# Kernel optimization log

Hardware: AMD Instinct MI355X
Metric: run time of the kernel (lower is better)

## Reference

```python
import jax, jax.numpy as jnp
import numpy as np

EPS = 1e-5
CLIP = 1.0

@jax.custom_vjp
def ste_sign(x):
    return jnp.sign(x)

def _ste_fwd(x):
    return jnp.sign(x), x

def _ste_bwd(x, g):
    return (g * (jnp.abs(x) <= CLIP).astype(g.dtype),)

ste_sign.defvjp(_ste_fwd, _ste_bwd)

def conv2d(x, w, stride, pad):
    return jax.lax.conv_general_dilated(
        x, w, window_strides=(stride, stride), padding=[(pad, pad), (pad, pad)],
        dimension_numbers=('NCHW', 'OIHW', 'NCHW'))

def bn(x, g, b, m, v):
    inv = g / jnp.sqrt(v + EPS)
    return x * inv[None, :, None, None] + (b - m * inv)[None, :, None, None]

def setup_inputs() -> dict:
    key = jax.random.key(0)
    ks = jax.random.split(key, 16)
    def rn(k, shape, scale=0.05):
        return jax.random.normal(k, shape, dtype=jnp.float32) * scale
    C = [64, 128, 128, 192, 192]
    d = {}
    d['x'] = jax.random.normal(ks[0], (128, 1, 128, 128), dtype=jnp.float32)
    d['conv1_w'] = rn(ks[1], (C[0], 1, 3, 3), 0.3)
    d['conv1_b'] = rn(ks[2], (C[0],))
    d['w2'] = rn(ks[3], (C[1], C[0], 3, 3), 0.3)
    d['w3'] = rn(ks[4], (C[2], C[1], 3, 3), 0.3)
    d['w4'] = rn(ks[5], (C[3], C[2], 3, 3), 0.3)
    d['w5'] = rn(ks[6], (C[4], C[3], 1, 1), 0.3)
    d['conv6_w'] = rn(ks[7], (12, C[4], 1, 1), 0.1)
    d['conv6_b'] = rn(ks[8], (12,))
    d['fc_w'] = rn(ks[9], (12, 12), 0.2)
    d['fc_b'] = rn(ks[10], (12,))
    for i, c in enumerate(C):
        kk = jax.random.split(jax.random.fold_in(key, 100 + i), 4)
        d[f'bn{i+1}_g'] = 1.0 + rn(kk[0], (c,), 0.1)
        d[f'bn{i+1}_b'] = rn(kk[1], (c,), 0.1)
        d[f'bn{i+1}_m'] = rn(kk[2], (c,), 0.1)
        d[f'bn{i+1}_v'] = 1.0 + jnp.abs(rn(kk[3], (c,), 0.1))
    return d

def reference(x, conv1_w, conv1_b, w2, w3, w4, w5, conv6_w, conv6_b, fc_w, fc_b,
              bn1_g, bn1_b, bn1_m, bn1_v, bn2_g, bn2_b, bn2_m, bn2_v,
              bn3_g, bn3_b, bn3_m, bn3_v, bn4_g, bn4_b, bn4_m, bn4_v,
              bn5_g, bn5_b, bn5_m, bn5_v):
    # conv1 (float) + BN + ReLU
    h = conv2d(x, conv1_w, 2, 1) + conv1_b[None, :, None, None]
    h = jax.nn.relu(bn(h, bn1_g, bn1_b, bn1_m, bn1_v))
    # binarized conv blocks: sign(activation) conv sign(weight)
    h = conv2d(ste_sign(h), ste_sign(w2), 1, 1)
    h = jax.nn.relu(bn(h, bn2_g, bn2_b, bn2_m, bn2_v))
    h = conv2d(ste_sign(h), ste_sign(w3), 2, 1)
    h = jax.nn.relu(bn(h, bn3_g, bn3_b, bn3_m, bn3_v))
    h = conv2d(ste_sign(h), ste_sign(w4), 1, 1)
    h = jax.nn.relu(bn(h, bn4_g, bn4_b, bn4_m, bn4_v))
    h = conv2d(ste_sign(h), ste_sign(w5), 1, 0)
    h = jax.nn.relu(bn(h, bn5_g, bn5_b, bn5_m, bn5_v))
    # 1x1 conv to classes, global average pool, FC, softmax
    h = conv2d(h, conv6_w, 1, 0) + conv6_b[None, :, None, None]
    h = jnp.mean(h, axis=(2, 3))  # [B, num_classes]
    logits = h @ fc_w.T + fc_b
    return jax.nn.softmax(logits, axis=1)
```

## Files before the change

### kernel.cpp

```cpp
#include <hip/hip_runtime.h>
#include <cstdint>

using u64 = unsigned long long;
using u32 = unsigned int;
typedef __attribute__((ext_vector_type(4))) int int4v;
typedef __attribute__((ext_vector_type(16))) int int16v;

struct PrepArgs {
  const float* bng[5]; const float* bnb[5]; const float* bnm[5]; const float* bnv[5];
  float* inv1; float* cc1; float* inv5; float* cc5;
  int* thr[3]; int* flp[3];
  const float* w[4];
  u64* wp[4]; u64* wz[4];
  u32* flags;
  const float* x; float* xpad;
  signed char* bf2x; signed char* bf3; signed char* bf4;
};

__device__ __forceinline__ void prep_all_body(const PrepArgs& a, int i) {
  if (i < 704) {
    const int off[6] = {0, 64, 192, 320, 512, 704};
    int l = 0;
    while (i >= off[l + 1]) ++l;
    int c = i - off[l];
    float iv = __fdiv_rn(a.bng[l][c], __fsqrt_rn(__fadd_rn(a.bnv[l][c], 1e-5f)));
    float cb = __fsub_rn(a.bnb[l][c], __fmul_rn(a.bnm[l][c], iv));
    if (l == 0) { a.inv1[c] = iv; a.cc1[c] = cb; }
    else if (l == 4) { a.inv5[c] = iv; a.cc5[c] = cb; }
    else {
      auto pred = [&](int v_) {
        return __fadd_rn(__fmul_rn((float)v_, iv), cb) > 0.f;
      };
      int Tx, fl;
      if (iv == 0.f) { Tx = pred(0) ? -100000 : 100000; fl = 0; }
      else if (iv > 0.f) {
        if (pred(-2048)) { Tx = -100000; fl = 0; }
        else if (!pred(2048)) { Tx = 100000; fl = 0; }
        else {
          int lo = -2048, hi = 2048;
          while (hi - lo > 1) { int md = (lo + hi) >> 1; if (pred(md)) hi = md; else lo = md; }
          Tx = hi; fl = 0;
        }
      } else {
        if (pred(2048)) { Tx = -100000; fl = -1; }
        else if (!pred(-2048)) { Tx = 100000; fl = -1; }
        else {
          int lo = -2048, hi = 2048;
          while (hi - lo > 1) { int md = (lo + hi) >> 1; if (pred(md)) lo = md; else hi = md; }
          Tx = lo ^ -1; fl = -1;
        }
      }
      a.thr[l - 1][c] = Tx; a.flp[l - 1][c] = fl;
    }
    return;
  }
  int j = i - 704;
  if (j >= 7488) return;
  const int poff[5] = {0, 1152, 3456, 6912, 7488};
  const int ICt[4] = {64, 128, 128, 192};
  const int Kt[4]  = {9, 9, 9, 1};
  const int Wt[4]  = {1, 2, 2, 3};
  int l = 0;
  while (j >= poff[l + 1]) ++l;
  int idx = j - poff[l];
  int W = Wt[l], K = Kt[l], IC = ICt[l];
  int wi = idx % W;
  int rest = idx / W;
  int t = rest % K;
  int oc = rest / K;
  u64 p = 0, z = 0;
  int icbase = wi * 64;
  int nb = IC - icbase; if (nb > 64) nb = 64;
  const float* w = a.w[l];
  for (int b = 0; b < nb; ++b) {
    float f = w[((size_t)oc * IC + (icbase + b)) * K + t];
    if (f > 0.f) p |= (1ull << b);
    else if (f == 0.f) z |= (1ull << b);
  }
  a.wp[l][idx] = p;
  a.wz[l][idx] = z;
  if (z) atomicOr(a.flags + l, 1u);
}

template <int CINW, int COUT>
__device__ __forceinline__ void prep_bfrag_body(const float* __restrict__ w,
                                                signed char* __restrict__ bf, int idx) {
  constexpr int NKC = 9 * CINW;
  constexpr int NT = COUT / 16;
  constexpr int CIN = 64 * CINW;
  if (idx >= NT * NKC * 64) return;
  int lane = idx & 63;
  int rest = idx >> 6;
  int kc = rest % NKC;
  int t = rest / NKC;
  int tap = kc / CINW, wd = kc % CINW;
  int n = t * 16 + (lane & 15);
  int icb = wd * 64 + (lane >> 4) * 16;
  signed char* dst = bf + (size_t)idx * 16;
#pragma unroll
  for (int i = 0; i < 16; ++i) {
    float f = w[((size_t)n * CIN + icb + i) * 9 + tap];
    dst[i] = (f > 0.f) ? 1 : ((f < 0.f) ? -1 : 0);
  }
}

__device__ __forceinline__ void prep_bfrag32_body(const float* __restrict__ w,
                                                  signed char* __restrict__ bf, int idx) {
  if (idx >= 4 * 18 * 64) return;
  int lane = idx & 63;
  int rest = idx >> 6;
  int s = rest % 18;
  int t = rest / 18;
  int oc = t * 32 + (lane & 31);
  int kbase = s * 32 + (lane >> 5) * 16;
  signed char* dst = bf + (size_t)idx * 16;
#pragma unroll
  for (int i = 0; i < 16; ++i) {
    int k = kbase + i;
    int ch = k & 63, tap = k >> 6;
    float f = w[((size_t)oc * 64 + ch) * 9 + tap];
    dst[i] = (f > 0.f) ? 1 : ((f < 0.f) ? -1 : 0);
  }
}

__global__ __launch_bounds__(256) void front(PrepArgs a) {
  int b = blockIdx.x, tid = threadIdx.x;
  if (b < 8192) {
    int idx = b * 256 + tid;
    int c = idx & 127, r = (idx >> 7) & 127, n = idx >> 14;
    a.xpad[((size_t)n * 130 + r + 1) * 136 + c + 1] = a.x[idx];
    return;
  }
  b -= 8192;
  if (b < 32) { prep_all_body(a, b * 256 + tid); return; }
  b -= 32;
  if (b < 18) { prep_bfrag32_body(a.w[0], a.bf2x, b * 256 + tid); return; }
  b -= 18;
  if (b < 36) { prep_bfrag_body<2, 128>(a.w[1], a.bf3, b * 256 + tid); return; }
  b -= 36;
  if (b < 54) { prep_bfrag_body<2, 192>(a.w[2], a.bf4, b * 256 + tid); return; }
}

__global__ __launch_bounds__(256) void conv1_bin(
    const float* __restrict__ xpad, const float* __restrict__ w1, const float* __restrict__ b1,
    const float* __restrict__ inv1, const float* __restrict__ cc1,
    u64* __restrict__ a1p) {
  int tid = threadIdx.x, lane = tid & 63;
  int rb = __builtin_amdgcn_readfirstlane(tid >> 6);
  int blk = blockIdx.x;
  int y = (blk % 16) * 4 + rb;
  int n = blk / 16;
  float W[9];
#pragma unroll
  for (int t = 0; t < 9; ++t) W[t] = w1[lane * 9 + t];
  float bias = b1[lane], iv = inv1[lane], cb = cc1[lane];
  const float* sb = xpad + ((size_t)n * 130 + 2 * y) * 136;
  float A[12], B[12], C[12];
  u64 rowm = 0;
  int xb = 0;

#define FLD(BUF, POFF)                                     \
  _Pragma("unroll") for (int _r = 0; _r < 3; ++_r)         \
  _Pragma("unroll") for (int _j = 0; _j < 4; ++_j)         \
    BUF[_r * 4 + _j] = sb[_r * 136 + (POFF) + _j];
#define FPX(XO, B0F, C0, B1F, C1, B2F, C2) {                          \
  float acc = 0.f;                                                    \
  _Pragma("unroll") for (int _r = 0; _r < 3; ++_r)                    \
    acc += B0F[_r * 4 + (C0)] * W[_r * 3 + 0]                         \
         + B1F[_r * 4 + (C1)] * W[_r * 3 + 1]                         \
         + B2F[_r * 4 + (C2)] * W[_r * 3 + 2];                        \
  float h = __fadd_rn(acc, bias);                                     \
  float bnv = __fadd_rn(__fmul_rn(h, iv), cb);                        \
  u64 _m = __ballot(bnv > 0.f);                                       \
  rowm = (lane == (XO)) ? _m : rowm; }
#define FSTEP(BA, BB, BC, POFF, XB)  \
  FLD(BC, (POFF) + 8);               \
  FPX((XB), BA, 0, BA, 1, BA, 2);    \
  FPX((XB) + 1, BA, 2, BA, 3, BB, 0);

  FLD(A, 0); FLD(B, 4);
  for (int g = 0; g < 10; ++g) {
    FSTEP(A, B, C, 0, xb);
    FSTEP(B, C, A, 4, xb + 2);
    FSTEP(C, A, B, 8, xb + 4);
    sb += 12; xb += 6;
  }
  FSTEP(A, B, C, 0, xb);
  FSTEP(B, C, A, 4, xb + 2);
  a1p[((size_t)n * 66 + (y + 1)) * 68 + lane + 1] = rowm;
#undef FLD
#undef FPX
#undef FSTEP
}

__global__ __launch_bounds__(256, 4) void bconv2_32(
    const u64* __restrict__ ain, const signed char* __restrict__ bf,
    const int* __restrict__ thr, const int* __restrict__ flp,
    u64* __restrict__ aout) {
  __shared__ int4v bs[2 * 18 * 64];
  int tid = threadIdx.x, lane = tid & 63;
  int wv = __builtin_amdgcn_readfirstlane(tid >> 6);
  int pos = blockIdx.x * 4 + wv;
  int xg = pos & 1;
  int y = (pos >> 1) & 63;
  int n = pos >> 7;
  int ln31 = lane & 31;
  int kg16 = (lane >> 5) * 16;
  int px = xg * 32 + ln31;

  const int4v* bfv = (const int4v*)bf;
  int4v breg[9];
#pragma unroll
  for (int i = 0; i < 9; ++i) breg[i] = bfv[tid + i * 256];

  const u64* abase = ain + ((size_t)n * 66 + y) * 68 + px;
  int4v af[18];
#pragma unroll
  for (int tap = 0; tap < 9; ++tap) {
    int dy = tap / 3, dx = tap % 3;
    u64 aw = abase[(size_t)dy * 68 + dx];
#pragma unroll
    for (int h = 0; h < 2; ++h) {
      u32 t16 = (u32)(aw >> (h * 32 + kg16)) & 0xFFFFu;
      int4v v;
      v.x = (int)((((t16      ) & 0xFu) * 0x00204081u) & 0x01010101u);
      v.y = (int)((((t16 >> 4 ) & 0xFu) * 0x00204081u) & 0x01010101u);
      v.z = (int)((((t16 >> 8 ) & 0xFu) * 0x00204081u) & 0x01010101u);
      v.w = (int)((((t16 >> 12) & 0xFu) * 0x00204081u) & 0x01010101u);
      af[tap * 2 + h] = v;
    }
  }

  int txv[4], flv[4];
#pragma unroll
  for (int t = 0; t < 4; ++t) { txv[t] = thr[t * 32 + ln31]; flv[t] = flp[t * 32 + ln31]; }

  u32* out32 = (u32*)aout;

#define C2_EPI(T, CREG) {                                             \
  int tx = txv[T], fl = flv[T];                                       \
  u32 oww = 0;                                                        \
  _Pragma("unroll") for (int r = 0; r < 16; ++r) {                    \
    int plo = (r & 3) + 8 * (r >> 2);                                 \
    u64 bal = __ballot((CREG[r] ^ fl) >= tx);                         \
    u32 wlo = (u32)bal, whi = (u32)(bal >> 32);                       \
    oww = (lane == plo) ? wlo : oww;                                  \
    oww = (lane == plo + 4) ? whi : oww;                              \
  }                                                                   \
  if (lane < 32) {                                                    \
    int xx = xg * 32 + lane;                                          \
    out32[(((size_t)n * 66 + (y + 1)) * 68 + (xx + 1)) * 4 + (T)] = oww; \
  } }

#pragma unroll
  for (int i = 0; i < 9; ++i) bs[tid + i * 256] = breg[i];
  __syncthreads();
#pragma unroll
  for (int i = 0; i < 9; ++i) breg[i] = bfv[2 * 18 * 64 + tid + i * 256];

#pragma unroll
  for (int t = 0; t < 2; ++t) {
    int16v c = {0, 0, 0, 0, 0, 0, 0, 0, 0, 0, 0, 0, 0, 0, 0, 0};
#pragma unroll
    for (int s = 0; s < 18; ++s) {
      int4v bb = bs[(t * 18 + s) * 64 + lane];
      c = __builtin_amdgcn_mfma_i32_32x32x32_i8(af[s], bb, c, 0, 0, 0);
    }
    C2_EPI(t, c)
  }

  __syncthreads();
#pragma unroll
  for (int i = 0; i < 9; ++i) bs[tid + i * 256] = breg[i];
  __syncthreads();
#pragma unroll
  for (int t = 2; t < 4; ++t) {
    int16v c = {0, 0, 0, 0, 0, 0, 0, 0, 0, 0, 0, 0, 0, 0, 0, 0};
#pragma unroll
    for (int s = 0; s < 18; ++s) {
      int4v bb = bs[((t - 2) * 18 + s) * 64 + lane];
      c = __builtin_amdgcn_mfma_i32_32x32x32_i8(af[s], bb, c, 0, 0, 0);
    }
    C2_EPI(t, c)
  }
#undef C2_EPI
}

template <int CINW, int COUT, int STRIDE, int IN_HW, int OUT_HW, int MT, int TSTG, int OPAD>
__global__ __launch_bounds__(256) void bconv_mfma(
    const u64* __restrict__ ain, const signed char* __restrict__ bf,
    const int* __restrict__ thr, const int* __restrict__ flp,
    u64* __restrict__ aout) {
  constexpr int IPW = IN_HW + 4;
  constexpr int NKC = 9 * CINW;
  constexpr int NT = COUT / 16;
  constexpr int NSTG = NT / TSTG;
  constexpr int OCW = (COUT + 63) / 64;
  constexpr int XG = OUT_HW / (16 * MT);
  constexpr int FRAG = TSTG * NKC * 64;
  constexpr int CPT = (FRAG + 255) / 256;
  constexpr int NW32 = NT / 2;
  __shared__ int4v bs[FRAG];

  int tid = threadIdx.x, lane = tid & 63;
  int wv = __builtin_amdgcn_readfirstlane(tid >> 6);
  int pos = blockIdx.x * 4 + wv;
  int xg = pos % XG;
  int rest = pos / XG;
  int y = rest % OUT_HW;
  int n = rest / OUT_HW;
  int m = lane & 15;
  int kg = lane >> 4;

  const int4v* bfv = (const int4v*)bf;

  int4v breg[CPT];
#pragma unroll
  for (int i = 0; i < CPT; ++i) {
    int ix = tid + i * 256;
    if (FRAG % 256 == 0 || ix < FRAG) breg[i] = bfv[ix];
  }

  int4v af[MT * NKC];
#pragma unroll
  for (int mt = 0; mt < MT; ++mt) {
    int x = (xg * MT + mt) * 16 + m;
    const u64* abase = ain + (((size_t)n * (IN_HW + 2) + STRIDE * y) * IPW
                              + (size_t)STRIDE * x) * CINW;
#pragma unroll
    for (int dy = 0; dy < 3; ++dy)
#pragma unroll
      for (int dx = 0; dx < 3; ++dx)
#pragma unroll
        for (int wd = 0; wd < CINW; ++wd) {
          u64 aw = abase[((size_t)dy * IPW + dx) * CINW + wd];
          u32 t16 = (u32)(aw >> (kg * 16)) & 0xFFFFu;
          int4v v;
          v.x = (int)((((t16      ) & 0xFu) * 0x00204081u) & 0x01010101u);
          v.y = (int)((((t16 >> 4 ) & 0xFu) * 0x00204081u) & 0x01010101u);
          v.z = (int)((((t16 >> 8 ) & 0xFu) * 0x00204081u) & 0x01010101u);
          v.w = (int)((((t16 >> 12) & 0xFu) * 0x00204081u) & 0x01010101u);
          af[mt * NKC + (dy * 3 + dx) * CINW + wd] = v;
        }
  }

  u32 acc32[MT][NW32];
#pragma unroll
  for (int mt = 0; mt < MT; ++mt)
#pragma unroll
    for (int wl = 0; wl < NW32; ++wl) acc32[mt][wl] = 0;

#pragma unroll
  for (int s = 0; s < NSTG; ++s) {
    __syncthreads();
#pragma unroll
    for (int i = 0; i < CPT; ++i) {
      int ix = tid + i * 256;
      if (FRAG % 256 == 0 || ix < FRAG) bs[ix] = breg[i];
    }
    __syncthreads();
    if (s + 1 < NSTG) {
      const int4v* src = bfv + (size_t)(s + 1) * FRAG;
#pragma unroll
      for (int i = 0; i < CPT; ++i) {
        int ix = tid + i * 256;
        if (FRAG % 256 == 0 || ix < FRAG) breg[i] = src[ix];
      }
    }
#pragma unroll
    for (int tl = 0; tl < TSTG; ++tl) {
      int4v c[MT];
#pragma unroll
      for (int mt = 0; mt < MT; ++mt) c[mt] = (int4v){0, 0, 0, 0};
#pragma unroll
      for (int kc = 0; kc < NKC; ++kc) {
        int4v bb = bs[(tl * NKC + kc) * 64 + lane];
#pragma unroll
        for (int mt = 0; mt < MT; ++mt)
          c[mt] = __builtin_amdgcn_mfma_i32_16x16x64_i8(af[mt * NKC + kc], bb, c[mt], 0, 0, 0);
      }
      const int t = s * TSTG + tl;
      int tx = thr[t * 16 + m];
      int fl = flp[t * 16 + m];
#pragma unroll
      for (int mt = 0; mt < MT; ++mt) {
        u64 b0 = __ballot((c[mt].x ^ fl) >= tx);
        u64 b1 = __ballot((c[mt].y ^ fl) >= tx);
        u64 b2 = __ballot((c[mt].z ^ fl) >= tx);
        u64 b3 = __ballot((c[mt].w ^ fl) >= tx);
        u64 s01 = (m & 1) ? b1 : b0;
        u64 s23 = (m & 1) ? b3 : b2;
        u64 bsel = (m & 2) ? s23 : s01;
        u32 slice = (u32)(bsel >> ((m >> 2) * 16)) & 0xFFFFu;
        acc32[mt][t >> 1] |= slice << ((t & 1) * 16);
      }
    }
  }

  if (kg == 0) {
    u32* out32 = (u32*)aout;
#pragma unroll
    for (int mt = 0; mt < MT; ++mt) {
      int x = (xg * MT + mt) * 16 + m;
      size_t px32;
      if (OPAD)
        px32 = (((size_t)n * (OUT_HW + 2) + (y + 1)) * (OUT_HW + 4) + (x + 1)) * (OCW * 2);
      else
        px32 = (((size_t)n * OUT_HW + y) * OUT_HW + x) * (OCW * 2);
#pragma unroll
      for (int wl = 0; wl < NW32; ++wl)
        out32[px32 + wl] = acc32[mt][wl];
    }
  }
}

#define NCH5 8
__global__ __launch_bounds__(192) void bconv5_pool(
    const u64* __restrict__ ain, const u64* __restrict__ wp, const u64* __restrict__ wz,
    const u32* __restrict__ flag, const float* __restrict__ inv5, const float* __restrict__ cc5,
    float* __restrict__ partial) {
  int n = blockIdx.x / NCH5, ch = blockIdx.x % NCH5;
  int oc = threadIdx.x;
  u64 W0 = wp[oc * 3], W1 = wp[oc * 3 + 1], W2 = wp[oc * 3 + 2];
  bool anyz = (*flag != 0u);
  float iv = inv5[oc], cb = cc5[oc];
  const u64* sb = ain + ((size_t)n * 1024 + ch * 128) * 3;
  u64 A0, A1, A2, B0, B1, B2, C0, C1, C2;
  float acc = 0.f;
#define LD5(P, a0_, a1_, a2_) { a0_ = sb[(P) * 3]; a1_ = sb[(P) * 3 + 1]; a2_ = sb[(P) * 3 + 2]; }
#define PX5(a0_, a1_, a2_) {                                                   \
  int _pa = __popcll(a0_) + __popcll(a1_) + __popcll(a2_);                     \
  int _s = __popcll(a0_ & W0) + __popcll(a1_ & W1) + __popcll(a2_ & W2);       \
  int _val = 2 * _s - _pa;                                                     \
  if (anyz) _val += __popcll(a0_ & wz[oc * 3]) + __popcll(a1_ & wz[oc * 3 + 1])\
                  + __popcll(a2_ & wz[oc * 3 + 2]);                            \
  float _b = __fadd_rn(__fmul_rn((float)_val, iv), cb);                        \
  acc += fmaxf(_b, 0.f); }
  LD5(0, A0, A1, A2); LD5(1, B0, B1, B2);
  for (int g = 0; g < 42; ++g) {
    LD5(2, C0, C1, C2); PX5(A0, A1, A2);
    LD5(3, A0, A1, A2); PX5(B0, B1, B2);
    LD5(4, B0, B1, B2); PX5(C0, C1, C2);
    sb += 9;
  }
  PX5(A0, A1, A2); PX5(B0, B1, B2);
  partial[((size_t)n * NCH5 + ch) * 192 + oc] = acc;
#undef LD5
#undef PX5
}

__global__ __launch_bounds__(192) void head2(
    const float* __restrict__ partial,
    const float* __restrict__ w6, const float* __restrict__ b6,
    const float* __restrict__ fw, const float* __restrict__ fb,
    float* __restrict__ out) {
  __shared__ float pool_s[192];
  __shared__ float h6s[12];
  __shared__ float lgs[12];
  int n = blockIdx.x, t = threadIdx.x;
  float s = 0.f;
#pragma unroll
  for (int ch = 0; ch < NCH5; ++ch) s += partial[((size_t)n * NCH5 + ch) * 192 + t];
  pool_s[t] = s;
  __syncthreads();
  if (t < 12) {
    float a = 0.f;
    for (int c = 0; c < 192; ++c) a += pool_s[c] * w6[t * 192 + c];
    h6s[t] = b6[t] + a * (1.0f / 1024.0f);
  }
  __syncthreads();
  if (t < 12) {
    float s2 = fb[t];
    for (int k = 0; k < 12; ++k) s2 += h6s[k] * fw[t * 12 + k];
    lgs[t] = s2;
  }
  __syncthreads();
  if (t == 0) {
    float mx = -1e30f;
    for (int j = 0; j < 12; ++j) mx = fmaxf(mx, lgs[j]);
    float e[12], se = 0.f;
    for (int j = 0; j < 12; ++j) { e[j] = expf(lgs[j] - mx); se += e[j]; }
    for (int j = 0; j < 12; ++j) out[n * 12 + j] = e[j] / se;
  }
}

extern "C" void kernel_launch(void* const* d_in, const int* in_sizes, int n_in,
                              void* d_out, int out_size, void* d_ws, size_t ws_size,
                              hipStream_t stream) {
  const float* x   = (const float*)d_in[0];
  const float* w1  = (const float*)d_in[1];
  const float* b1  = (const float*)d_in[2];
  const float* w2  = (const float*)d_in[3];
  const float* w3  = (const float*)d_in[4];
  const float* w4  = (const float*)d_in[5];
  const float* w5  = (const float*)d_in[6];
  const float* w6  = (const float*)d_in[7];
  const float* b6  = (const float*)d_in[8];
  const float* fcw = (const float*)d_in[9];
  const float* fcb = (const float*)d_in[10];
  float* out = (float*)d_out;

  char* ws = (char*)d_ws;
  size_t off = 0;
  auto alloc = [&](size_t bytes) -> void* {
    void* p = ws + off;
    off += (bytes + 255) & ~(size_t)255;
    return p;
  };
  size_t xp_sz = (size_t)128 * 130 * 136 * 4;
  size_t a1_sz = (size_t)128 * 66 * 68 * 1 * 8;
  size_t a2_sz = (size_t)128 * 66 * 68 * 2 * 8;
  size_t a3_sz = (size_t)128 * 34 * 36 * 2 * 8;
  float* xpad = (float*)alloc(xp_sz);
  u64* a1p = (u64*)alloc(a1_sz);
  u64* a2p = (u64*)alloc(a2_sz);
  u64* a3p = (u64*)alloc(a3_sz);
  size_t zero_sz = xp_sz + a1_sz + a2_sz + a3_sz;
  u64* a4p = (u64*)alloc((size_t)128 * 32 * 32 * 3 * 8);
  float* partial = (float*)alloc((size_t)128 * NCH5 * 192 * 4);
  float* inv1 = (float*)alloc(64 * 4);
  float* cc1  = (float*)alloc(64 * 4);
  float* inv5 = (float*)alloc(192 * 4);
  float* cc5  = (float*)alloc(192 * 4);
  int* thr2 = (int*)alloc(128 * 4); int* flp2 = (int*)alloc(128 * 4);
  int* thr3 = (int*)alloc(128 * 4); int* flp3 = (int*)alloc(128 * 4);
  int* thr4 = (int*)alloc(192 * 4); int* flp4 = (int*)alloc(192 * 4);
  u64* wp2 = (u64*)alloc(128 * 9 * 1 * 8);
  u64* wz2 = (u64*)alloc(128 * 9 * 1 * 8);
  u64* wp3 = (u64*)alloc(128 * 9 * 2 * 8);
  u64* wz3 = (u64*)alloc(128 * 9 * 2 * 8);
  u64* wp4 = (u64*)alloc(192 * 9 * 2 * 8);
  u64* wz4 = (u64*)alloc(192 * 9 * 2 * 8);
  u64* wp5 = (u64*)alloc(192 * 1 * 3 * 8);
  u64* wz5 = (u64*)alloc(192 * 1 * 3 * 8);
  u32* flags = (u32*)alloc(4 * sizeof(u32));
  signed char* bf2x = (signed char*)alloc((size_t)4 * 18 * 64 * 16);
  signed char* bf3 = (signed char*)alloc((size_t)8 * 18 * 64 * 16);
  signed char* bf4 = (signed char*)alloc((size_t)12 * 18 * 64 * 16);
  (void)ws_size; (void)n_in; (void)in_sizes; (void)out_size;

  hipMemsetAsync(xpad, 0, zero_sz, stream);
  hipMemsetAsync(flags, 0, 4 * sizeof(u32), stream);

  PrepArgs pa;
  for (int l = 0; l < 5; ++l) {
    pa.bng[l] = (const float*)d_in[11 + 4 * l + 0];
    pa.bnb[l] = (const float*)d_in[11 + 4 * l + 1];
    pa.bnm[l] = (const float*)d_in[11 + 4 * l + 2];
    pa.bnv[l] = (const float*)d_in[11 + 4 * l + 3];
  }
  pa.inv1 = inv1; pa.cc1 = cc1; pa.inv5 = inv5; pa.cc5 = cc5;
  pa.thr[0] = thr2; pa.flp[0] = flp2;
  pa.thr[1] = thr3; pa.flp[1] = flp3;
  pa.thr[2] = thr4; pa.flp[2] = flp4;
  pa.w[0] = w2; pa.w[1] = w3; pa.w[2] = w4; pa.w[3] = w5;
  pa.wp[0] = wp2; pa.wp[1] = wp3; pa.wp[2] = wp4; pa.wp[3] = wp5;
  pa.wz[0] = wz2; pa.wz[1] = wz3; pa.wz[2] = wz4; pa.wz[3] = wz5;
  pa.flags = flags;
  pa.x = x; pa.xpad = xpad;
  pa.bf2x = bf2x; pa.bf3 = bf3; pa.bf4 = bf4;

  front<<<8192 + 32 + 18 + 36 + 54, 256, 0, stream>>>(pa);

  conv1_bin<<<128 * 16, 256, 0, stream>>>(xpad, w1, b1, inv1, cc1, a1p);

  bconv2_32<<<4096, 256, 0, stream>>>(a1p, bf2x, thr2, flp2, a2p);

  bconv_mfma<2, 128, 2, 64, 32, 1, 1, 1><<<2048, 256, 0, stream>>>(
      a2p, bf3, thr3, flp3, a3p);

  bconv_mfma<2, 192, 1, 32, 32, 1, 1, 0><<<2048, 256, 0, stream>>>(
      a3p, bf4, thr4, flp4, a4p);

  bconv5_pool<<<128 * NCH5, 192, 0, stream>>>(a4p, wp5, wz5, flags + 3, inv5, cc5, partial);

  head2<<<128, 192, 0, stream>>>(partial, w6, b6, fcw, fcb, out);
}
```

Measured before the change: 201.3 us.

## Switch conv3/conv4 to 32x32x32 int8 MFMA with double-buffered weight tiles

Replaces the 16x16x64 MFMA binary conv kernel for layers 3 and 4 with a 32x32x32 int8 MFMA kernel where each wave handles a full 32-pixel output row. The weight fragments are repacked into a new 32-wide layout and staged through double-buffered shared memory, one output tile per iteration. The epilogue packs the ballot-based binarisation into 32-bit words per tile. This halves the block count and aims to improve MFMA efficiency and reuse of activation fragments, at the cost of more registers (36 A fragments) and a larger shared buffer that may reduce occupancy.

```diff
diff --git a/kernel.cpp b/kernel.cpp
--- a/kernel.cpp
+++ b/kernel.cpp
@@ -82,28 +82,6 @@
   if (z) atomicOr(a.flags + l, 1u);
 }
 
-template <int CINW, int COUT>
-__device__ __forceinline__ void prep_bfrag_body(const float* __restrict__ w,
-                                                signed char* __restrict__ bf, int idx) {
-  constexpr int NKC = 9 * CINW;
-  constexpr int NT = COUT / 16;
-  constexpr int CIN = 64 * CINW;
-  if (idx >= NT * NKC * 64) return;
-  int lane = idx & 63;
-  int rest = idx >> 6;
-  int kc = rest % NKC;
-  int t = rest / NKC;
-  int tap = kc / CINW, wd = kc % CINW;
-  int n = t * 16 + (lane & 15);
-  int icb = wd * 64 + (lane >> 4) * 16;
-  signed char* dst = bf + (size_t)idx * 16;
-#pragma unroll
-  for (int i = 0; i < 16; ++i) {
-    float f = w[((size_t)n * CIN + icb + i) * 9 + tap];
-    dst[i] = (f > 0.f) ? 1 : ((f < 0.f) ? -1 : 0);
-  }
-}
-
 __device__ __forceinline__ void prep_bfrag32_body(const float* __restrict__ w,
                                                   signed char* __restrict__ bf, int idx) {
   if (idx >= 4 * 18 * 64) return;
@@ -123,6 +101,27 @@
   }
 }
 
+template <int COUT>
+__device__ __forceinline__ void prep_bfrag32b_body(const float* __restrict__ w,
+                                                   signed char* __restrict__ bf, int idx) {
+  constexpr int NT = COUT / 32;
+  if (idx >= NT * 36 * 64) return;
+  int lane = idx & 63;
+  int rest = idx >> 6;
+  int s = rest % 36;
+  int t = rest / 36;
+  int oc = t * 32 + (lane & 31);
+  int kbase = s * 32 + (lane >> 5) * 16;
+  signed char* dst = bf + (size_t)idx * 16;
+#pragma unroll
+  for (int i = 0; i < 16; ++i) {
+    int k = kbase + i;
+    int ch = k % 128, tap = k / 128;
+    float f = w[((size_t)oc * 128 + ch) * 9 + tap];
+    dst[i] = (f > 0.f) ? 1 : ((f < 0.f) ? -1 : 0);
+  }
+}
+
 __global__ __launch_bounds__(256) void front(PrepArgs a) {
   int b = blockIdx.x, tid = threadIdx.x;
   if (b < 8192) {
@@ -136,9 +135,9 @@
   b -= 32;
   if (b < 18) { prep_bfrag32_body(a.w[0], a.bf2x, b * 256 + tid); return; }
   b -= 18;
-  if (b < 36) { prep_bfrag_body<2, 128>(a.w[1], a.bf3, b * 256 + tid); return; }
+  if (b < 36) { prep_bfrag32b_body<128>(a.w[1], a.bf3, b * 256 + tid); return; }
   b -= 36;
-  if (b < 54) { prep_bfrag_body<2, 192>(a.w[2], a.bf4, b * 256 + tid); return; }
+  if (b < 54) { prep_bfrag32b_body<192>(a.w[2], a.bf4, b * 256 + tid); return; }
 }
 
 __global__ __launch_bounds__(256) void conv1_bin(
@@ -286,131 +285,86 @@
 #undef C2_EPI
 }
 
-template <int CINW, int COUT, int STRIDE, int IN_HW, int OUT_HW, int MT, int TSTG, int OPAD>
-__global__ __launch_bounds__(256) void bconv_mfma(
+template <int COUT, int STRIDE, int IN_HW, int OPAD>
+__global__ __launch_bounds__(256) void bconv34_32(
     const u64* __restrict__ ain, const signed char* __restrict__ bf,
     const int* __restrict__ thr, const int* __restrict__ flp,
     u64* __restrict__ aout) {
   constexpr int IPW = IN_HW + 4;
-  constexpr int NKC = 9 * CINW;
-  constexpr int NT = COUT / 16;
-  constexpr int NSTG = NT / TSTG;
-  constexpr int OCW = (COUT + 63) / 64;
-  constexpr int XG = OUT_HW / (16 * MT);
-  constexpr int FRAG = TSTG * NKC * 64;
-  constexpr int CPT = (FRAG + 255) / 256;
-  constexpr int NW32 = NT / 2;
-  __shared__ int4v bs[FRAG];
-
+  constexpr int NT = COUT / 32;
+  constexpr int TW = 36 * 64;
+  constexpr int OW32 = COUT / 32;
+  __shared__ int4v bs[2][TW];
   int tid = threadIdx.x, lane = tid & 63;
   int wv = __builtin_amdgcn_readfirstlane(tid >> 6);
   int pos = blockIdx.x * 4 + wv;
-  int xg = pos % XG;
-  int rest = pos / XG;
-  int y = rest % OUT_HW;
-  int n = rest / OUT_HW;
-  int m = lane & 15;
-  int kg = lane >> 4;
+  int y = pos & 31;
+  int n = pos >> 5;
+  int ln31 = lane & 31;
+  int h = lane >> 5;
 
   const int4v* bfv = (const int4v*)bf;
 
-  int4v breg[CPT];
-#pragma unroll
-  for (int i = 0; i < CPT; ++i) {
-    int ix = tid + i * 256;
-    if (FRAG % 256 == 0 || ix < FRAG) breg[i] = bfv[ix];
-  }
-
-  int4v af[MT * NKC];
-#pragma unroll
-  for (int mt = 0; mt < MT; ++mt) {
-    int x = (xg * MT + mt) * 16 + m;
-    const u64* abase = ain + (((size_t)n * (IN_HW + 2) + STRIDE * y) * IPW
-                              + (size_t)STRIDE * x) * CINW;
-#pragma unroll
-    for (int dy = 0; dy < 3; ++dy)
-#pragma unroll
-      for (int dx = 0; dx < 3; ++dx)
-#pragma unroll
-        for (int wd = 0; wd < CINW; ++wd) {
-          u64 aw = abase[((size_t)dy * IPW + dx) * CINW + wd];
-          u32 t16 = (u32)(aw >> (kg * 16)) & 0xFFFFu;
-          int4v v;
-          v.x = (int)((((t16      ) & 0xFu) * 0x00204081u) & 0x01010101u);
-          v.y = (int)((((t16 >> 4 ) & 0xFu) * 0x00204081u) & 0x01010101u);
-          v.z = (int)((((t16 >> 8 ) & 0xFu) * 0x00204081u) & 0x01010101u);
-          v.w = (int)((((t16 >> 12) & 0xFu) * 0x00204081u) & 0x01010101u);
-          af[mt * NKC + (dy * 3 + dx) * CINW + wd] = v;
-        }
-  }
-
-  u32 acc32[MT][NW32];
-#pragma unroll
-  for (int mt = 0; mt < MT; ++mt)
-#pragma unroll
-    for (int wl = 0; wl < NW32; ++wl) acc32[mt][wl] = 0;
-
-#pragma unroll
-  for (int s = 0; s < NSTG; ++s) {
+  const u64* abase = ain + (((size_t)n * (IN_HW + 2) + (size_t)STRIDE * y) * IPW
+                            + (size_t)STRIDE * ln31) * 2;
+  int4v af[36];
+#pragma unroll
+  for (int tap = 0; tap < 9; ++tap) {
+    int dy = tap / 3, dx = tap % 3;
+    u64 w0 = abase[((size_t)dy * IPW + dx) * 2 + 0];
+    u64 w1 = abase[((size_t)dy * IPW + dx) * 2 + 1];
+#pragma unroll
+    for (int q = 0; q < 4; ++q) {
+      int m2 = 2 * q + h;
+      u64 aw = (m2 & 4) ? w1 : w0;
+      int sh = (m2 & 3) * 16;
+      u32 t16 = (u32)(aw >> sh) & 0xFFFFu;
+      int4v v;
+      v.x = (int)((((t16      ) & 0xFu) * 0x00204081u) & 0x01010101u);
+      v.y = (int)((((t16 >> 4 ) & 0xFu) * 0x00204081u) & 0x01010101u);
+      v.z = (int)((((t16 >> 8 ) & 0xFu) * 0x00204081u) & 0x01010101u);
+      v.w = (int)((((t16 >> 12) & 0xFu) * 0x00204081u) & 0x01010101u);
+      af[tap * 4 + q] = v;
+    }
+  }
+
+#pragma unroll
+  for (int i = 0; i < 9; ++i) bs[0][tid + i * 256] = bfv[tid + i * 256];
+  __syncthreads();
+
+  u32* out32 = (u32*)aout;
+  size_t px32;
+  if (OPAD)
+    px32 = (((size_t)n * 34 + (y + 1)) * 36 + (ln31 + 1)) * OW32;
+  else
+    px32 = (((size_t)n * 32 + y) * 32 + ln31) * OW32;
+
+#pragma unroll 1
+  for (int t = 0; t < NT; ++t) {
+    if (t + 1 < NT) {
+      const int4v* src = bfv + (size_t)(t + 1) * TW;
+#pragma unroll
+      for (int i = 0; i < 9; ++i) bs[(t + 1) & 1][tid + i * 256] = src[tid + i * 256];
+    }
+    int16v c = {0, 0, 0, 0, 0, 0, 0, 0, 0, 0, 0, 0, 0, 0, 0, 0};
+#pragma unroll
+    for (int s = 0; s < 36; ++s) {
+      int4v bb = bs[t & 1][s * 64 + lane];
+      c = __builtin_amdgcn_mfma_i32_32x32x32_i8(af[s], bb, c, 0, 0, 0);
+    }
+    int tx = thr[t * 32 + ln31];
+    int fl = flp[t * 32 + ln31];
+    u32 oww = 0;
+#pragma unroll
+    for (int r = 0; r < 16; ++r) {
+      int plo = (r & 3) + 8 * (r >> 2);
+      u64 bal = __ballot((c[r] ^ fl) >= tx);
+      u32 wlo = (u32)bal, whi = (u32)(bal >> 32);
+      oww = (lane == plo) ? wlo : oww;
+      oww = (lane == plo + 4) ? whi : oww;
+    }
+    if (lane < 32) out32[px32 + t] = oww;
     __syncthreads();
-#pragma unroll
-    for (int i = 0; i < CPT; ++i) {
-      int ix = tid + i * 256;
-      if (FRAG % 256 == 0 || ix < FRAG) bs[ix] = breg[i];
-    }
-    __syncthreads();
-    if (s + 1 < NSTG) {
-      const int4v* src = bfv + (size_t)(s + 1) * FRAG;
-#pragma unroll
-      for (int i = 0; i < CPT; ++i) {
-        int ix = tid + i * 256;
-        if (FRAG % 256 == 0 || ix < FRAG) breg[i] = src[ix];
-      }
-    }
-#pragma unroll
-    for (int tl = 0; tl < TSTG; ++tl) {
-      int4v c[MT];
-#pragma unroll
-      for (int mt = 0; mt < MT; ++mt) c[mt] = (int4v){0, 0, 0, 0};
-#pragma unroll
-      for (int kc = 0; kc < NKC; ++kc) {
-        int4v bb = bs[(tl * NKC + kc) * 64 + lane];
-#pragma unroll
-        for (int mt = 0; mt < MT; ++mt)
-          c[mt] = __builtin_amdgcn_mfma_i32_16x16x64_i8(af[mt * NKC + kc], bb, c[mt], 0, 0, 0);
-      }
-      const int t = s * TSTG + tl;
-      int tx = thr[t * 16 + m];
-      int fl = flp[t * 16 + m];
-#pragma unroll
-      for (int mt = 0; mt < MT; ++mt) {
-        u64 b0 = __ballot((c[mt].x ^ fl) >= tx);
-        u64 b1 = __ballot((c[mt].y ^ fl) >= tx);
-        u64 b2 = __ballot((c[mt].z ^ fl) >= tx);
-        u64 b3 = __ballot((c[mt].w ^ fl) >= tx);
-        u64 s01 = (m & 1) ? b1 : b0;
-        u64 s23 = (m & 1) ? b3 : b2;
-        u64 bsel = (m & 2) ? s23 : s01;
-        u32 slice = (u32)(bsel >> ((m >> 2) * 16)) & 0xFFFFu;
-        acc32[mt][t >> 1] |= slice << ((t & 1) * 16);
-      }
-    }
-  }
-
-  if (kg == 0) {
-    u32* out32 = (u32*)aout;
-#pragma unroll
-    for (int mt = 0; mt < MT; ++mt) {
-      int x = (xg * MT + mt) * 16 + m;
-      size_t px32;
-      if (OPAD)
-        px32 = (((size_t)n * (OUT_HW + 2) + (y + 1)) * (OUT_HW + 4) + (x + 1)) * (OCW * 2);
-      else
-        px32 = (((size_t)n * OUT_HW + y) * OUT_HW + x) * (OCW * 2);
-#pragma unroll
-      for (int wl = 0; wl < NW32; ++wl)
-        out32[px32 + wl] = acc32[mt][wl];
-    }
   }
 }
 
@@ -535,8 +489,8 @@
   u64* wz5 = (u64*)alloc(192 * 1 * 3 * 8);
   u32* flags = (u32*)alloc(4 * sizeof(u32));
   signed char* bf2x = (signed char*)alloc((size_t)4 * 18 * 64 * 16);
-  signed char* bf3 = (signed char*)alloc((size_t)8 * 18 * 64 * 16);
-  signed char* bf4 = (signed char*)alloc((size_t)12 * 18 * 64 * 16);
+  signed char* bf3 = (signed char*)alloc((size_t)4 * 36 * 64 * 16);
+  signed char* bf4 = (signed char*)alloc((size_t)6 * 36 * 64 * 16);
   (void)ws_size; (void)n_in; (void)in_sizes; (void)out_size;
 
   hipMemsetAsync(xpad, 0, zero_sz, stream);
@@ -566,10 +520,10 @@
 
   bconv2_32<<<4096, 256, 0, stream>>>(a1p, bf2x, thr2, flp2, a2p);
 
-  bconv_mfma<2, 128, 2, 64, 32, 1, 1, 1><<<2048, 256, 0, stream>>>(
+  bconv34_32<128, 2, 64, 1><<<1024, 256, 0, stream>>>(
       a2p, bf3, thr3, flp3, a3p);
 
-  bconv_mfma<2, 192, 1, 32, 32, 1, 1, 0><<<2048, 256, 0, stream>>>(
+  bconv34_32<192, 1, 32, 0><<<1024, 256, 0, stream>>>(
       a3p, bf4, thr4, flp4, a4p);
 
   bconv5_pool<<<128 * NCH5, 192, 0, stream>>>(a4p, wp5, wz5, flags + 3, inv5, cc5, partial);
```

Result: faster. 184.3 us, median of 2 (-8.4%).
